# Optimization experiments

Measured on AMD Instinct MI355X. Metric: run time of the kernel, lower is better.

Reference implementation:

```python
import jax, jax.numpy as jnp
import numpy as np

N_VOICES = 8
N_PROFILES = 16
N_HARMONICS = 64
N_FRAMES = 64
N_SAMPLES = 2 ** 14  # 16384
SAMPLERATE = 22050
NYQUIST = SAMPLERATE / 2.0
MIN_FREQ = 40.0 / NYQUIST
# Reproduces the source's chained assignment `self.freq_interval = self.max_freq = self.min_freq`
FREQ_INTERVAL = MIN_FREQ
RATIOS = (np.arange(2, 2 + N_HARMONICS).astype(np.float32)) ** 2  # [64]


def _interp_linear(x, out_size):
    """torch F.interpolate(mode='linear', align_corners=False) along last axis."""
    n = x.shape[-1]
    scale = n / out_size
    coords = (jnp.arange(out_size, dtype=x.dtype) + 0.5) * scale - 0.5
    coords = jnp.clip(coords, 0.0, n - 1)
    lo = jnp.floor(coords).astype(jnp.int32)
    hi = jnp.minimum(lo + 1, n - 1)
    w = (coords - lo.astype(x.dtype))
    return x[..., lo] * (1.0 - w) + x[..., hi] * w


def setup_inputs() -> dict:
    key = jax.random.key(0)
    k1, k2, k3 = jax.random.split(key, 3)
    f0 = jax.random.normal(k1, (16, N_VOICES * 2, N_FRAMES), dtype=jnp.float32)
    harmonics = jax.random.normal(k2, (16, N_VOICES * N_PROFILES, N_FRAMES), dtype=jnp.float32)
    profiles = jax.random.uniform(k3, (N_PROFILES, N_HARMONICS), dtype=jnp.float32, minval=0.0, maxval=0.1)
    return {"f0": f0, "harmonics": harmonics, "profiles": profiles}


def reference(f0, harmonics, profiles):
    b = f0.shape[0]
    f0 = f0.reshape(b, N_VOICES, 2, N_FRAMES)
    harm = harmonics.reshape(b, N_VOICES, N_PROFILES, N_FRAMES)

    re, im = f0[:, :, 0, :], f0[:, :, 1, :]
    f0_amp = re * re + im * im                      # ||.||^2 over dim=-2, [b,v,f]
    ang = jnp.arctan2(im, re) / jnp.pi              # torch.angle(complex)/pi
    base = MIN_FREQ + (ang * ang) * FREQ_INTERVAL   # [b,v,f]

    ratios = jnp.asarray(RATIOS)
    hfreq = jnp.clip(base[:, :, None, :] * ratios[None, None, :, None], 0.0, 1.0)  # [b,v,h,f]

    w = jax.nn.softmax(harm, axis=2)                # softmax over profiles
    hamp = jnp.einsum('bvpf,ph->bvhf', w, profiles)
    hamp = jnp.clip(hamp, 0.0, 1.0) * f0_amp[:, :, None, :]

    full_freq = jnp.concatenate([base[:, :, None, :], hfreq], axis=2)
    full_amp = jnp.concatenate([f0_amp[:, :, None, :], hamp], axis=2)
    full_freq = full_freq.reshape(b * N_VOICES, N_HARMONICS + 1, N_FRAMES)
    full_amp = full_amp.reshape(b * N_VOICES, N_HARMONICS + 1, N_FRAMES)

    ff = _interp_linear(full_freq, N_SAMPLES)       # [b*v, 65, 16384]
    fa = _interp_linear(full_amp, N_SAMPLES)

    sig = fa * jnp.sin(jnp.cumsum(ff, axis=-1) * jnp.pi)
    sig = sig.reshape(b, N_VOICES, N_HARMONICS + 1, N_SAMPLES).sum(axis=(1, 2))
    return sig.reshape(b, 1, N_SAMPLES)
```

## Files before the change

### kernel.cpp

```cpp
#include <hip/hip_runtime.h>
#include <math.h>

#define NVOICE 8
#define NPROF  16
#define NHARM  64
#define NFRAME 64
#define NSAMP  16384
#define NB     16

#define NKEEP  16
#define NROWS2 (NVOICE * NKEEP)

typedef float f32x2 __attribute__((ext_vector_type(2)));
typedef float f32x4 __attribute__((ext_vector_type(4)));

__device__ __forceinline__ float min_freq() { return 40.0f / 11025.0f; }
__device__ __forceinline__ f32x4 sp4(float s) { return (f32x4){s, s, s, s}; }

__global__ __launch_bounds__(256)
void hm_fused(const float* __restrict__ f0,
              const float* __restrict__ harm,
              const float* __restrict__ prof,
              float* __restrict__ out)
{
    const int blk = blockIdx.x;
    const int b   = blk >> 4;
    const int qd  = blk & 15;
    const int c0  = qd * 4;
    const int c3  = c0 + 3;
    const int tid = threadIdx.x;

    __shared__ float  sBase[NVOICE][NFRAME + 1];
    __shared__ float  sAmp0[NVOICE][NFRAME + 1];
    __shared__ float  sProf[NPROF][NKEEP];
    __shared__ float  sW[NVOICE][6][NPROF];
    __shared__ float  sP[5][NROWS2];
    __shared__ float  sA[6][NROWS2];
    __shared__ float4 cf[4][2][NROWS2];
    __shared__ f32x2  pf2[4][2][NROWS2 / 2];

    sProf[tid >> 4][tid & 15] = prof[(tid >> 4) * NHARM + (tid & 15)];

    for (int idx = tid; idx < NVOICE * NFRAME; idx += 256) {
        const int v = idx >> 6, k = idx & 63;
        const float re  = f0[((size_t)b * 16 + 2 * v    ) * NFRAME + k];
        const float im  = f0[((size_t)b * 16 + 2 * v + 1) * NFRAME + k];
        const float ang = atan2f(im, re) * 0.3183098861837907f;
        sBase[v][k] = min_freq() + ang * ang * min_freq();
        sAmp0[v][k] = re * re + im * im;
    }
    __syncthreads();

    if (tid < NROWS2) {
        const int r = tid, v = r >> 4, h = r & 15;
        const float r2 = (float)((h + 1) * (h + 1));
        if (c0 == 0) sP[0][r] = 0.0f;
        double p = 0.0;
        float prevF = 0.0f;
        for (int k = 0; k <= c3; ++k) {
            const float F = fminf(sBase[v][k] * r2, 1.0f);
            p += 64.0 * (double)(prevF + F);
            prevF = F;
            const int fi = k - (c0 - 1);
            if (fi >= 0) sP[fi][r] = (float)(p - floor(p));
        }
    } else if (tid < 128 + 48) {
        const int t2 = tid - 128;
        const int v = t2 / 6, fi = t2 % 6;
        const int f = min(max(c0 - 1 + fi, 0), 63);
        float w[NPROF];
        float m = -INFINITY;
#pragma unroll
        for (int p = 0; p < NPROF; ++p) {
            w[p] = harm[((size_t)b * (NVOICE * NPROF) + v * NPROF + p) * NFRAME + f];
            m = fmaxf(m, w[p]);
        }
        float s = 0.0f;
#pragma unroll
        for (int p = 0; p < NPROF; ++p) { w[p] = expf(w[p] - m); s += w[p]; }
        const float inv = 1.0f / s;
#pragma unroll
        for (int p = 0; p < NPROF; ++p) sW[v][fi][p] = w[p] * inv;
    }
    __syncthreads();

    for (int idx = tid; idx < 6 * NROWS2; idx += 256) {
        const int fi = idx >> 7, r = idx & 127, v = r >> 4, h = r & 15;
        const int f = min(max(c0 - 1 + fi, 0), 63);
        const float a0 = sAmp0[v][f];
        float A = a0;
        if (h != 0) {
            float d = 0.0f;
#pragma unroll
            for (int p = 0; p < NPROF; ++p) d = fmaf(sW[v][fi][p], sProf[p][h - 1], d);
            A = fminf(fmaxf(d, 0.0f), 1.0f) * a0;
        }
        sA[fi][r] = A;
    }
    __syncthreads();

    for (int idx = tid; idx < 8 * NROWS2; idx += 256) {
        const int qh = idx >> 7, r = idx & 127;
        const int q = qh >> 1, hh = qh & 1;
        const int v = r >> 4, h = r & 15;
        const float r2 = (float)((h + 1) * (h + 1));
        const int fiA = q + hh, fiB = fiA + 1;
        const int fA = min(max(c0 - 1 + fiA, 0), 63);
        const int fB = min(max(c0 - 1 + fiB, 0), 63);
        const float Fa = 0.5f * fminf(sBase[v][fA] * r2, 1.0f);
        const float Fb = 0.5f * fminf(sBase[v][fB] * r2, 1.0f);
        const float Aa = sA[fiA][r], Ab = sA[fiB][r];
        cf[q][hh][r] = make_float4(Fa, Fb - Fa, Aa, Ab - Aa);
        ((float*)pf2[q][hh])[r] = hh ? sP[q + 1][r] : sP[q][r];
    }
    __syncthreads();

    const int q    = tid >> 6;
    const int lane = tid & 63;
    const int h    = lane >> 5;
    const int l    = lane & 31;
    const int c    = c0 + q;

    f32x4 t1, t2, t3;
#pragma unroll
    for (int u = 0; u < 4; ++u) {
        const int j = l + 32 * u + (h ? 0 : 128);
        float t1v = (float)(j + 1);
        if (c == 0 && h == 0) t1v = (float)(l + 32 * u + 1);
        t1[u] = t1v;
        t2[u] = (float)((j + 1) * (j + 1)) * (1.0f / 512.0f);
        t3[u] = ((float)j + 0.5f) * (1.0f / 256.0f);
    }

    const float4* __restrict__ V  = cf[q][h];
    const f32x2*  __restrict__ Pp = pf2[q][h];

    f32x4 acc = {0.0f, 0.0f, 0.0f, 0.0f};
#pragma unroll 4
    for (int g = 0; g < NROWS2 / 2; ++g) {
        const f32x2  pp = Pp[g];
        const float4 v0 = V[2 * g];
        const float4 v1 = V[2 * g + 1];
        {
            const f32x4 x  = __builtin_elementwise_fma(t2, sp4(v0.y),
                                 __builtin_elementwise_fma(t1, sp4(v0.x), sp4(pp.x)));
            const f32x4 fa = __builtin_elementwise_fma(t3, sp4(v0.w), sp4(v0.z));
            const f32x4 sn = {
                __builtin_amdgcn_sinf(__builtin_amdgcn_fractf(x[0])),
                __builtin_amdgcn_sinf(__builtin_amdgcn_fractf(x[1])),
                __builtin_amdgcn_sinf(__builtin_amdgcn_fractf(x[2])),
                __builtin_amdgcn_sinf(__builtin_amdgcn_fractf(x[3])) };
            acc = __builtin_elementwise_fma(fa, sn, acc);
        }
        {
            const f32x4 x  = __builtin_elementwise_fma(t2, sp4(v1.y),
                                 __builtin_elementwise_fma(t1, sp4(v1.x), sp4(pp.y)));
            const f32x4 fa = __builtin_elementwise_fma(t3, sp4(v1.w), sp4(v1.z));
            const f32x4 sn = {
                __builtin_amdgcn_sinf(__builtin_amdgcn_fractf(x[0])),
                __builtin_amdgcn_sinf(__builtin_amdgcn_fractf(x[1])),
                __builtin_amdgcn_sinf(__builtin_amdgcn_fractf(x[2])),
                __builtin_amdgcn_sinf(__builtin_amdgcn_fractf(x[3])) };
            acc = __builtin_elementwise_fma(fa, sn, acc);
        }
    }

    float* o = out + (size_t)b * NSAMP + c * 256 + (h ? 128 : 0) + l;
    o[0]  = acc[0];
    o[32] = acc[1];
    o[64] = acc[2];
    o[96] = acc[3];
}

extern "C" void kernel_launch(void* const* d_in, const int* in_sizes, int n_in,
                              void* d_out, int out_size, void* d_ws, size_t ws_size,
                              hipStream_t stream)
{
    const float* f0   = (const float*)d_in[0];
    const float* harm = (const float*)d_in[1];
    const float* prof = (const float*)d_in[2];

    hm_fused<<<NB * 16, 256, 0, stream>>>(f0, harm, prof, (float*)d_out);
}
```

Baseline: 16.87 us.

## Pack per-row coefficients into half2 records and recompute frequencies in the inner loop

The per-row coefficient table shrinks from a float4 plus a float phase to one uint4 holding two rows. Each row keeps its amplitude and amplitude slope as packed fp16 and its phase as fp32. Frequency terms are no longer stored but recomputed in the main loop from per-voice base values and constant harmonic ratios, which cuts LDS traffic per sinusoid. The serial double-precision phase prefix sum is also unrolled by four for frames before the tile. The cost is fp16 rounding on amplitudes, a few extra VALU ops per row, and the loss of the explicit f32x4 vector packing.

```diff
diff --git a/kernel.cpp b/kernel.cpp
--- a/kernel.cpp
+++ b/kernel.cpp
@@ -1,4 +1,5 @@
 #include <hip/hip_runtime.h>
+#include <hip/hip_fp16.h>
 #include <math.h>
 
 #define NVOICE 8
@@ -11,11 +12,9 @@
 #define NKEEP  16
 #define NROWS2 (NVOICE * NKEEP)
 
-typedef float f32x2 __attribute__((ext_vector_type(2)));
-typedef float f32x4 __attribute__((ext_vector_type(4)));
-
 __device__ __forceinline__ float min_freq() { return 40.0f / 11025.0f; }
-__device__ __forceinline__ f32x4 sp4(float s) { return (f32x4){s, s, s, s}; }
+
+union U32H2 { unsigned u; __half2 h; };
 
 __global__ __launch_bounds__(256)
 void hm_fused(const float* __restrict__ f0,
@@ -30,16 +29,16 @@
     const int c3  = c0 + 3;
     const int tid = threadIdx.x;
 
-    __shared__ float  sBase[NVOICE][NFRAME + 1];
-    __shared__ float  sAmp0[NVOICE][NFRAME + 1];
-    __shared__ float  sProf[NPROF][NKEEP];
-    __shared__ float  sW[NVOICE][6][NPROF];
-    __shared__ float  sP[5][NROWS2];
-    __shared__ float  sA[6][NROWS2];
-    __shared__ float4 cf[4][2][NROWS2];
-    __shared__ f32x2  pf2[4][2][NROWS2 / 2];
+    __shared__ float sBase[NVOICE][NFRAME];
+    __shared__ float sAmp0[NVOICE][NFRAME];
+    __shared__ float sProf[NPROF][NKEEP];
+    __shared__ float sW[NVOICE][6][NPROF];
+    __shared__ float sPP[5][NROWS2];
+    __shared__ float sA[6][NROWS2];
+    __shared__ uint4 pr[4][2][NROWS2 / 2];
 
     sProf[tid >> 4][tid & 15] = prof[(tid >> 4) * NHARM + (tid & 15)];
+    if (c0 == 0 && tid < NROWS2) sPP[0][tid] = 0.0f;
 
     for (int idx = tid; idx < NVOICE * NFRAME; idx += 256) {
         const int v = idx >> 6, k = idx & 63;
@@ -52,21 +51,34 @@
     __syncthreads();
 
     if (tid < NROWS2) {
-        const int r = tid, v = r >> 4, h = r & 15;
-        const float r2 = (float)((h + 1) * (h + 1));
-        if (c0 == 0) sP[0][r] = 0.0f;
+        const int r = tid, v = r >> 4, hh = r & 15;
+        const float r2 = (float)((hh + 1) * (hh + 1));
         double p = 0.0;
         float prevF = 0.0f;
-        for (int k = 0; k <= c3; ++k) {
+        int k = 0;
+        const int kb = max(0, c0 - 1) & ~3;
+        for (; k < kb; k += 4) {
+            const float Fa = fminf(sBase[v][k    ] * r2, 1.0f);
+            const float Fb = fminf(sBase[v][k + 1] * r2, 1.0f);
+            const float Fc = fminf(sBase[v][k + 2] * r2, 1.0f);
+            const float Fd = fminf(sBase[v][k + 3] * r2, 1.0f);
+            const double t0 = (double)(prevF + Fa);
+            const double t1 = (double)(Fa + Fb);
+            const double t2 = (double)(Fb + Fc);
+            const double t3 = (double)(Fc + Fd);
+            p += 64.0 * ((t0 + t1) + (t2 + t3));
+            prevF = Fd;
+        }
+        for (; k <= c3; ++k) {
             const float F = fminf(sBase[v][k] * r2, 1.0f);
             p += 64.0 * (double)(prevF + F);
             prevF = F;
             const int fi = k - (c0 - 1);
-            if (fi >= 0) sP[fi][r] = (float)(p - floor(p));
+            if (fi >= 0) sPP[fi][r] = (float)(p - floor(p));
         }
     } else if (tid < 128 + 48) {
-        const int t2 = tid - 128;
-        const int v = t2 / 6, fi = t2 % 6;
+        const int t = tid - 128;
+        const int v = t / 6, fi = t % 6;
         const int f = min(max(c0 - 1 + fi, 0), 63);
         float w[NPROF];
         float m = -INFINITY;
@@ -85,33 +97,35 @@
     __syncthreads();
 
     for (int idx = tid; idx < 6 * NROWS2; idx += 256) {
-        const int fi = idx >> 7, r = idx & 127, v = r >> 4, h = r & 15;
+        const int fi = idx >> 7, r = idx & 127, v = r >> 4, hh = r & 15;
         const int f = min(max(c0 - 1 + fi, 0), 63);
         const float a0 = sAmp0[v][f];
         float A = a0;
-        if (h != 0) {
+        if (hh != 0) {
             float d = 0.0f;
 #pragma unroll
-            for (int p = 0; p < NPROF; ++p) d = fmaf(sW[v][fi][p], sProf[p][h - 1], d);
+            for (int p = 0; p < NPROF; ++p) d = fmaf(sW[v][fi][p], sProf[p][hh - 1], d);
             A = fminf(fmaxf(d, 0.0f), 1.0f) * a0;
         }
         sA[fi][r] = A;
     }
     __syncthreads();
 
-    for (int idx = tid; idx < 8 * NROWS2; idx += 256) {
-        const int qh = idx >> 7, r = idx & 127;
-        const int q = qh >> 1, hh = qh & 1;
-        const int v = r >> 4, h = r & 15;
-        const float r2 = (float)((h + 1) * (h + 1));
-        const int fiA = q + hh, fiB = fiA + 1;
-        const int fA = min(max(c0 - 1 + fiA, 0), 63);
-        const int fB = min(max(c0 - 1 + fiB, 0), 63);
-        const float Fa = 0.5f * fminf(sBase[v][fA] * r2, 1.0f);
-        const float Fb = 0.5f * fminf(sBase[v][fB] * r2, 1.0f);
-        const float Aa = sA[fiA][r], Ab = sA[fiB][r];
-        cf[q][hh][r] = make_float4(Fa, Fb - Fa, Aa, Ab - Aa);
-        ((float*)pf2[q][hh])[r] = hh ? sP[q + 1][r] : sP[q][r];
+    for (int idx = tid; idx < 8 * (NROWS2 / 2); idx += 256) {
+        const int qh = idx >> 6, g = idx & 63;
+        const int q = qh >> 1, hh2 = qh & 1;
+        const int fiA = q + hh2, fiB = fiA + 1;
+        const int r0 = 2 * g, r1 = 2 * g + 1;
+        const float Aa0 = sA[fiA][r0], Ad0 = sA[fiB][r0] - Aa0;
+        const float Aa1 = sA[fiA][r1], Ad1 = sA[fiB][r1] - Aa1;
+        U32H2 u0; u0.h = __floats2half2_rn(Aa0, Ad0);
+        U32H2 u1; u1.h = __floats2half2_rn(Aa1, Ad1);
+        uint4 rec;
+        rec.x = u0.u;
+        rec.y = __float_as_uint(sPP[fiA][r0]);
+        rec.z = u1.u;
+        rec.w = __float_as_uint(sPP[fiA][r1]);
+        pr[q][hh2][g] = rec;
     }
     __syncthreads();
 
@@ -121,7 +135,7 @@
     const int l    = lane & 31;
     const int c    = c0 + q;
 
-    f32x4 t1, t2, t3;
+    float t1[4], t2[4], t3[4];
 #pragma unroll
     for (int u = 0; u < 4; ++u) {
         const int j = l + 32 * u + (h ? 0 : 128);
@@ -132,36 +146,50 @@
         t3[u] = ((float)j + 0.5f) * (1.0f / 256.0f);
     }
 
-    const float4* __restrict__ V  = cf[q][h];
-    const f32x2*  __restrict__ Pp = pf2[q][h];
-
-    f32x4 acc = {0.0f, 0.0f, 0.0f, 0.0f};
-#pragma unroll 4
-    for (int g = 0; g < NROWS2 / 2; ++g) {
-        const f32x2  pp = Pp[g];
-        const float4 v0 = V[2 * g];
-        const float4 v1 = V[2 * g + 1];
-        {
-            const f32x4 x  = __builtin_elementwise_fma(t2, sp4(v0.y),
-                                 __builtin_elementwise_fma(t1, sp4(v0.x), sp4(pp.x)));
-            const f32x4 fa = __builtin_elementwise_fma(t3, sp4(v0.w), sp4(v0.z));
-            const f32x4 sn = {
-                __builtin_amdgcn_sinf(__builtin_amdgcn_fractf(x[0])),
-                __builtin_amdgcn_sinf(__builtin_amdgcn_fractf(x[1])),
-                __builtin_amdgcn_sinf(__builtin_amdgcn_fractf(x[2])),
-                __builtin_amdgcn_sinf(__builtin_amdgcn_fractf(x[3])) };
-            acc = __builtin_elementwise_fma(fa, sn, acc);
-        }
-        {
-            const f32x4 x  = __builtin_elementwise_fma(t2, sp4(v1.y),
-                                 __builtin_elementwise_fma(t1, sp4(v1.x), sp4(pp.y)));
-            const f32x4 fa = __builtin_elementwise_fma(t3, sp4(v1.w), sp4(v1.z));
-            const f32x4 sn = {
-                __builtin_amdgcn_sinf(__builtin_amdgcn_fractf(x[0])),
-                __builtin_amdgcn_sinf(__builtin_amdgcn_fractf(x[1])),
-                __builtin_amdgcn_sinf(__builtin_amdgcn_fractf(x[2])),
-                __builtin_amdgcn_sinf(__builtin_amdgcn_fractf(x[3])) };
-            acc = __builtin_elementwise_fma(fa, sn, acc);
+    const int fA = min(max(c - 1 + h, 0), 63);
+    const int fB = min(c + h, 63);
+    const uint4* __restrict__ R = pr[q][h];
+
+    float acc[4] = {0.0f, 0.0f, 0.0f, 0.0f};
+#pragma unroll 2
+    for (int v = 0; v < NVOICE; ++v) {
+        const float bA = sBase[v][fA];
+        const float bB = sBase[v][fB];
+#pragma unroll
+        for (int hp = 0; hp < 8; ++hp) {
+            const uint4 rec = R[v * 8 + hp];
+            const float c2a = 0.5f * (float)((2 * hp + 1) * (2 * hp + 1));
+            const float c2b = 0.5f * (float)((2 * hp + 2) * (2 * hp + 2));
+            {
+                const float F2a = fminf(bA * c2a, 0.5f);
+                const float dF2 = fminf(bB * c2a, 0.5f) - F2a;
+                U32H2 cv; cv.u = rec.x;
+                const float A  = __low2float(cv.h);
+                const float dA = __high2float(cv.h);
+                const float P2 = __uint_as_float(rec.y);
+#pragma unroll
+                for (int u = 0; u < 4; ++u) {
+                    const float x  = fmaf(t2[u], dF2, fmaf(t1[u], F2a, P2));
+                    const float fa = fmaf(t3[u], dA, A);
+                    acc[u] = fmaf(fa,
+                        __builtin_amdgcn_sinf(__builtin_amdgcn_fractf(x)), acc[u]);
+                }
+            }
+            {
+                const float F2a = fminf(bA * c2b, 0.5f);
+                const float dF2 = fminf(bB * c2b, 0.5f) - F2a;
+                U32H2 cv; cv.u = rec.z;
+                const float A  = __low2float(cv.h);
+                const float dA = __high2float(cv.h);
+                const float P2 = __uint_as_float(rec.w);
+#pragma unroll
+                for (int u = 0; u < 4; ++u) {
+                    const float x  = fmaf(t2[u], dF2, fmaf(t1[u], F2a, P2));
+                    const float fa = fmaf(t3[u], dA, A);
+                    acc[u] = fmaf(fa,
+                        __builtin_amdgcn_sinf(__builtin_amdgcn_fractf(x)), acc[u]);
+                }
+            }
         }
     }
 
```

After: 16.98 us. Within noise of the previous version (+0.6%).
